# Kernel tuning notes

Measured on AMD Instinct MI355X. Metric: run time of the kernel, lower is better.

The kernel has to match this reference:

```python
import jax, jax.numpy as jnp
import numpy as np

BETA = 0.25

def _l2norm(x, eps=1e-12):
    # F.normalize(x, dim=-1)
    n = jnp.sqrt(jnp.sum(x * x, axis=-1, keepdims=True))
    return x / jnp.maximum(n, eps)

def setup_inputs() -> dict:
    key = jax.random.key(0)
    k1, k2 = jax.random.split(key)
    z = jax.random.normal(k1, (32, 1024, 32), dtype=jnp.float32)
    embedding = jax.random.normal(k2, (8192, 32), dtype=jnp.float32)
    return {"z": z, "embedding": embedding}

def reference(z, embedding):
    B, T, D = z.shape
    zf = _l2norm(z.reshape(-1, D))            # [N, D]
    en = _l2norm(embedding)                   # [n_e, D]
    # squared distances: ||z||^2 + ||e||^2 - 2 z.e  -> [N, n_e]
    d = (jnp.sum(zf * zf, axis=1, keepdims=True)
         + jnp.sum(en * en, axis=1)
         - 2.0 * jnp.einsum('nd,kd->nk', zf, en))
    idx = jnp.argmin(d, axis=1).reshape(B, T)            # [B, T]
    z_q = embedding[idx]                                  # [B, T, D] gather
    z_qnorm = _l2norm(z_q)
    z_norm = _l2norm(z)
    loss = (BETA * jnp.mean((jax.lax.stop_gradient(z_qnorm) - z_norm) ** 2)
            + jnp.mean((z_qnorm - jax.lax.stop_gradient(z_norm)) ** 2))
    # straight-through estimator
    z_q_out = z + jax.lax.stop_gradient(z_qnorm - z)
    return z_q_out, loss, idx
```

## Files before the change

### kernel.cpp

```cpp
#include <hip/hip_runtime.h>
#include <math.h>


#define D 32
#define KCODES 8192
#define MARGIN_Q 5.0e-4f
#define EPS 1e-12f

typedef short bf16x8 __attribute__((ext_vector_type(8)));
typedef unsigned short u16x8 __attribute__((ext_vector_type(8)));
typedef float f32x4 __attribute__((ext_vector_type(4)));

static __device__ __forceinline__ unsigned short f2bf(float x) {
  unsigned u = __float_as_uint(x);
  return (unsigned short)((u + 0x7FFFu + ((u >> 16) & 1u)) >> 16);
}
static __device__ __forceinline__ float bf2f(unsigned short s) {
  return __uint_as_float(((unsigned)s) << 16);
}
static __device__ __forceinline__ void gload_lds16(const void* g, void* l) {
  __builtin_amdgcn_global_load_lds(
      (const __attribute__((address_space(1))) void*)g,
      (__attribute__((address_space(3))) void*)l, 16, 0, 0);
}


__global__ __launch_bounds__(256) void k_prep(const float* __restrict__ emb,
                                              float* __restrict__ en,
                                              float* __restrict__ en_h,
                                              unsigned short* __restrict__ eswz,
                                              int* __restrict__ cnt,
                                              float* __restrict__ loss) {
  int v = blockIdx.x * 256 + threadIdx.x;
  if (v == 0) { *cnt = 0; *loss = 0.f; }
  if (v >= KCODES) return;

  float x[D];
  const float4* p = reinterpret_cast<const float4*>(emb + (size_t)v * D);
#pragma unroll
  for (int j = 0; j < D / 4; ++j) {
    float4 q = p[j];
    x[4 * j + 0] = q.x; x[4 * j + 1] = q.y; x[4 * j + 2] = q.z; x[4 * j + 3] = q.w;
  }
  float ss = 0.f;
#pragma unroll
  for (int j = 0; j < D; ++j) ss = fmaf(x[j], x[j], ss);
  float n = fmaxf(sqrtf(ss), EPS);
#pragma unroll
  for (int j = 0; j < D; ++j) x[j] = x[j] / n;

  float4* o = reinterpret_cast<float4*>(en + (size_t)v * D);
  float s2 = 0.f;
#pragma unroll
  for (int j = 0; j < D / 4; ++j) {
    float4 q = {x[4 * j], x[4 * j + 1], x[4 * j + 2], x[4 * j + 3]};
    s2 = fmaf(q.x, q.x, fmaf(q.y, q.y, fmaf(q.z, q.z, fmaf(q.w, q.w, s2))));
    o[j] = q;
  }
  en_h[v] = 0.5f * s2;

  unsigned short hi[D], lo[D];
#pragma unroll
  for (int j = 0; j < D; ++j) {
    hi[j] = f2bf(x[j]);
    lo[j] = f2bf(x[j] - bf2f(hi[j]));
  }
  int tl = v >> 4, m = v & 15;
#pragma unroll
  for (int q = 0; q < 4; ++q) {
    u16x8 hv, lv;
#pragma unroll
    for (int j = 0; j < 8; ++j) { hv[j] = hi[8 * q + j]; lv[j] = lo[8 * q + j]; }
    *(u16x8*)(eswz + (size_t)tl * 1024 + (q * 16 + m) * 8) = hv;
    *(u16x8*)(eswz + (size_t)tl * 1024 + 512 + (q * 16 + m) * 8) = lv;
  }
}

__global__ __launch_bounds__(256, 2) void k_argmin_mfma(
    const float* __restrict__ z,
    const unsigned short* __restrict__ eswz,
    int* __restrict__ idx_ws, int* __restrict__ list, int* __restrict__ cnt,
    unsigned long long* __restrict__ mp2) {
  __shared__ unsigned short lds_sh[2][16384];

  const int tid = threadIdx.x;
  const int wid = tid >> 6, lane = tid & 63;
  const int lane15 = lane & 15, quad = lane >> 4;
  const int g = blockIdx.x * 4 + wid;

  const float4* gall = reinterpret_cast<const float4*>(eswz);
#pragma unroll
  for (int i = 0; i < 8; ++i) {
    int off = i * 256 + tid;
    gload_lds16(gall + off, (char*)&lds_sh[0][0] + (size_t)off * 16);
  }

  bf16x8 zhi, zlo;
  {
    const float4* p = reinterpret_cast<const float4*>(z + (size_t)(g * 16 + lane15) * D);
    float ss = 0.f;
#pragma unroll
    for (int j = 0; j < 8; ++j) {
      float4 q = p[j];
      ss = fmaf(q.x, q.x, fmaf(q.y, q.y, fmaf(q.z, q.z, fmaf(q.w, q.w, ss))));
    }
    float nn = fmaxf(sqrtf(ss), EPS);
    float4 a0 = p[quad * 2], a1 = p[quad * 2 + 1];
    float xs[8] = {a0.x / nn, a0.y / nn, a0.z / nn, a0.w / nn,
                   a1.x / nn, a1.y / nn, a1.z / nn, a1.w / nn};
#pragma unroll
    for (int j = 0; j < 8; ++j) {
      unsigned short h = f2bf(xs[j]);
      zhi[j] = (short)h;
      zlo[j] = (short)f2bf(xs[j] - bf2f(h));
    }
  }

  unsigned p1[4], p2[4];
#pragma unroll
  for (int r = 0; r < 4; ++r) { p1[r] = 0u; p2[r] = 0u; }
  const f32x4 initA = {1.25f, 1.25f, 1.25f, 1.25f};
  const f32x4 zero4 = {0.f, 0.f, 0.f, 0.f};

  for (int c = 0; c < 32; ++c) {
    __syncthreads();
    if (c + 1 < 32) {
      const float4* gn = gall + (size_t)(c + 1) * 2048;
      char* dst = (char*)&lds_sh[(c + 1) & 1][0];
#pragma unroll
      for (int i = 0; i < 8; ++i) {
        int off = i * 256 + tid;
        gload_lds16(gn + off, dst + (size_t)off * 16);
      }
    }
    const unsigned short* buf = &lds_sh[c & 1][0];
    bf16x8 cbh = *(const bf16x8*)(buf + lane * 8);
    bf16x8 cbl = *(const bf16x8*)(buf + 512 + lane * 8);
    const unsigned tbase = (unsigned)(511 - c * 16);
#pragma unroll
    for (int t = 0; t < 16; ++t) {
      bf16x8 nbh, nbl;
      if (t < 15) {
        nbh = *(const bf16x8*)(buf + (t + 1) * 1024 + lane * 8);
        nbl = *(const bf16x8*)(buf + (t + 1) * 1024 + 512 + lane * 8);
      }
      f32x4 aa = __builtin_amdgcn_mfma_f32_16x16x32_bf16(zhi, cbh, initA, 0, 0, 0);
      f32x4 ab = __builtin_amdgcn_mfma_f32_16x16x32_bf16(zhi, cbl, zero4, 0, 0, 0);
      ab = __builtin_amdgcn_mfma_f32_16x16x32_bf16(zlo, cbh, ab, 0, 0, 0);
      const unsigned tid9 = tbase - t;
#pragma unroll
      for (int r = 0; r < 4; ++r) {
        float sa = aa[r] + ab[r];
        unsigned pk = (__float_as_uint(sa) & 0xFFFFFE00u) | tid9;
        unsigned tmin = (pk < p1[r]) ? pk : p1[r];
        p1[r] = (pk > p1[r]) ? pk : p1[r];
        p2[r] = (tmin > p2[r]) ? tmin : p2[r];
      }
      cbh = nbh; cbl = nbl;
    }
  }

#pragma unroll
  for (int r = 0; r < 4; ++r) {
    int kl = (511 - (int)(p1[r] & 511u)) * 16 + lane15;
    unsigned sb = p1[r] & 0xFFFFFE00u;
    float s1f = __uint_as_float(sb);
    float s2f = __uint_as_float(p2[r] & 0xFFFFFE00u);
    unsigned long long pk =
        ((unsigned long long)sb << 32) | (unsigned)(8191 - kl);
#pragma unroll
    for (int m = 1; m <= 8; m <<= 1) {
      unsigned long long op = __shfl_xor(pk, m, 64);
      float os1 = __shfl_xor(s1f, m, 64);
      float os2 = __shfl_xor(s2f, m, 64);
      s2f = fmaxf(fmaxf(s2f, os2), fminf(s1f, os1));
      s1f = fmaxf(s1f, os1);
      pk = (op > pk) ? op : pk;
    }
    if (lane15 == 0) {
      int orow = g * 16 + quad * 4 + r;
      if (s1f - s2f < MARGIN_Q) {
        int pos = atomicAdd(cnt, 1);
        list[pos] = orow;
        mp2[pos] = 0ull;
        idx_ws[orow] = -(pos + 1);
      } else {
        idx_ws[orow] = 8191 - (int)(unsigned)(pk & 0xFFFFFFFFull);
      }
    }
  }
}

__global__ __launch_bounds__(256) void k_cleanup(const float* __restrict__ z,
                                                 const float* __restrict__ en,
                                                 const float* __restrict__ en_h,
                                                 const int* __restrict__ list,
                                                 const int* __restrict__ cnt,
                                                 unsigned long long* __restrict__ mp2) {
  __shared__ unsigned long long wred[4];
  const int tid = threadIdx.x;
  const int lane = tid & 63, wid = tid >> 6;
  const int ntask = (*cnt) * 32;

  for (int j = blockIdx.x; j < ntask; j += gridDim.x) {
    int i = j >> 5, kc = j & 31;
    int row = list[i];
    const float* zr = z + (size_t)row * D;
    float v[D];
    float ss = 0.f;
#pragma unroll
    for (int d = 0; d < D; ++d) v[d] = zr[d];
#pragma unroll
    for (int d = 0; d < D; ++d) ss = fmaf(v[d], v[d], ss);
    float n = fmaxf(sqrtf(ss), EPS);
#pragma unroll
    for (int d = 0; d < D; ++d) v[d] = v[d] / n;

    int k = kc * 256 + tid;
    const float4* er = reinterpret_cast<const float4*>(en + (size_t)k * D);
    float a = -en_h[k];
#pragma unroll
    for (int jj = 0; jj < 8; ++jj) {
      float4 e = er[jj];
      a = fmaf(v[4 * jj + 0], e.x, a);
      a = fmaf(v[4 * jj + 1], e.y, a);
      a = fmaf(v[4 * jj + 2], e.z, a);
      a = fmaf(v[4 * jj + 3], e.w, a);
    }
    unsigned o = __float_as_uint(a);
    o = (o & 0x80000000u) ? ~o : (o | 0x80000000u);
    unsigned long long pk = ((unsigned long long)o << 32) | (unsigned)(8191 - k);
#pragma unroll
    for (int m = 32; m >= 1; m >>= 1) {
      unsigned long long op = __shfl_xor(pk, m, 64);
      pk = (op > pk) ? op : pk;
    }
    if (lane == 0) wred[wid] = pk;
    __syncthreads();
    if (tid == 0) {
      unsigned long long m01 = (wred[0] > wred[1]) ? wred[0] : wred[1];
      unsigned long long m23 = (wred[2] > wred[3]) ? wred[2] : wred[3];
      atomicMax(&mp2[i], (m01 > m23) ? m01 : m23);
    }
    __syncthreads();
  }
}

__global__ __launch_bounds__(256) void k_epi(const float* __restrict__ z,
                                             const float* __restrict__ en,
                                             const int* __restrict__ idx_ws,
                                             const unsigned long long* __restrict__ mp2,
                                             float* __restrict__ out_z,
                                             float* __restrict__ loss,
                                             float* __restrict__ out_idx,
                                             float scale) {
  int row = blockIdx.x * 256 + threadIdx.x;
  int kb = idx_ws[row];
  if (kb < 0) {
    unsigned long long m = mp2[-kb - 1];
    kb = 8191 - (int)(unsigned)(m & 0xFFFFFFFFull);
  }
  out_idx[row] = (float)kb;

  const float4* p = reinterpret_cast<const float4*>(z + (size_t)row * D);
  float4 q[D / 4];
#pragma unroll
  for (int j = 0; j < D / 4; ++j) q[j] = p[j];
  float ss = 0.f;
#pragma unroll
  for (int j = 0; j < D / 4; ++j)
    ss = fmaf(q[j].x, q[j].x, fmaf(q[j].y, q[j].y, fmaf(q[j].z, q[j].z, fmaf(q[j].w, q[j].w, ss))));
  float n = fmaxf(sqrtf(ss), EPS);

  const float4* ep = reinterpret_cast<const float4*>(en + (size_t)kb * D);
  float4* op = reinterpret_cast<float4*>(out_z + (size_t)row * D);
  float s = 0.f;
#pragma unroll
  for (int j = 0; j < D / 4; ++j) {
    float4 e = ep[j];
    float4 o;
    o.x = q[j].x + (e.x - q[j].x);
    o.y = q[j].y + (e.y - q[j].y);
    o.z = q[j].z + (e.z - q[j].z);
    o.w = q[j].w + (e.w - q[j].w);
    op[j] = o;
    float dx = e.x - q[j].x / n;  float dy = e.y - q[j].y / n;
    float dz = e.z - q[j].z / n;  float dw = e.w - q[j].w / n;
    s = fmaf(dx, dx, fmaf(dy, dy, fmaf(dz, dz, fmaf(dw, dw, s))));
  }

#pragma unroll
  for (int off = 32; off > 0; off >>= 1) s += __shfl_down(s, off, 64);
  __shared__ float wsum[4];
  int lane = threadIdx.x & 63, wid = threadIdx.x >> 6;
  if (lane == 0) wsum[wid] = s;
  __syncthreads();
  if (threadIdx.x == 0) {
    float tt = (wsum[0] + wsum[1]) + (wsum[2] + wsum[3]);
    atomicAdd(loss, tt * scale);
  }
}

extern "C" void kernel_launch(void* const* d_in, const int* in_sizes, int n_in,
                              void* d_out, int out_size, void* d_ws, size_t ws_size,
                              hipStream_t stream) {
  const float* z = (const float*)d_in[0];
  const float* emb = (const float*)d_in[1];
  const int N = in_sizes[0] / D;
  const int K = in_sizes[1] / D;

  float* out = (float*)d_out;
  float* out_z = out;
  float* loss = out + (size_t)N * D;
  float* out_idx = out + (size_t)N * D + 1;

  char* w = (char*)d_ws;
  float* en = (float*)w;                         w += (size_t)K * D * 4;
  float* en_h = (float*)w;                       w += (size_t)K * 4;
  unsigned short* eswz = (unsigned short*)w;     w += (size_t)K * D * 2 * 2;
  int* idx_ws = (int*)w;                         w += (size_t)N * 4;
  int* list = (int*)w;                           w += (size_t)N * 4;
  unsigned long long* mp2 = (unsigned long long*)w; w += (size_t)N * 8;
  int* cnt = (int*)w;

  k_prep<<<dim3(K / 256), 256, 0, stream>>>(emb, en, en_h, eswz, cnt, loss);

  k_argmin_mfma<<<dim3(N / 64), 256, 0, stream>>>(
      z, eswz, idx_ws, list, cnt, mp2);

  k_cleanup<<<dim3(2048), 256, 0, stream>>>(z, en, en_h, list, cnt, mp2);

  k_epi<<<dim3(N / 256), 256, 0, stream>>>(
      z, en, idx_ws, mp2, out_z, loss, out_idx, 1.25f / (float)((size_t)N * D));
}
```

Baseline: 210.0 us.

## Split codebook across blocks, reuse codebook tiles over four row groups per wave

The argmin kernel now splits the 8192 codes into 4 slices along a second grid dimension, and each wave handles 64 rows (four 16-row MFMA groups) against each LDS-loaded codebook tile. The goal is to amortise the LDS reads and global loads of the codebook across more rows and to fuse the MFMA accumulation into a single chain. Partial top-2 results are written per split, and the last-arriving block for a row group (found with an atomic ticket counter) merges them and flags ambiguous rows. The cleanup margin is tightened and the packed index uses fewer bits. The change adds some workspace traffic, more registers per wave and dead leftover code, and a tighter margin raises the risk of incorrect argmins.

```diff
diff --git a/kernel.cpp b/kernel.cpp
--- a/kernel.cpp
+++ b/kernel.cpp
@@ -4,7 +4,11 @@
 
 #define D 32
 #define KCODES 8192
-#define MARGIN_Q 5.0e-4f
+#define KSPLIT 4
+#define SPLITCODES 2048
+#define NCHUNK 8
+#define MASK8 0xFFFFFF00u
+#define MARGIN_Q 2.0e-4f
 #define EPS 1e-12f
 
 typedef short bf16x8 __attribute__((ext_vector_type(8)));
@@ -22,6 +26,9 @@
   __builtin_amdgcn_global_load_lds(
       (const __attribute__((address_space(1))) void*)g,
       (__attribute__((address_space(3))) void*)l, 16, 0, 0);
+}
+static __device__ __forceinline__ unsigned umax3(unsigned a, unsigned b, unsigned c) {
+  return max(max(a, b), c);
 }
 
 
@@ -30,9 +37,12 @@
                                               float* __restrict__ en_h,
                                               unsigned short* __restrict__ eswz,
                                               int* __restrict__ cnt,
-                                              float* __restrict__ loss) {
+                                              float* __restrict__ loss,
+                                              int* __restrict__ tick,
+                                              int ntick) {
   int v = blockIdx.x * 256 + threadIdx.x;
   if (v == 0) { *cnt = 0; *loss = 0.f; }
+  if (v < ntick) tick[v] = 0;
   if (v >= KCODES) return;
 
   float x[D];
@@ -79,25 +89,35 @@
 __global__ __launch_bounds__(256, 2) void k_argmin_mfma(
     const float* __restrict__ z,
     const unsigned short* __restrict__ eswz,
+    unsigned long long* __restrict__ mpp,
+    float* __restrict__ g2,
+    int* __restrict__ tick,
     int* __restrict__ idx_ws, int* __restrict__ list, int* __restrict__ cnt,
-    unsigned long long* __restrict__ mp2) {
+    unsigned long long* __restrict__ mp2, int N) {
   __shared__ unsigned short lds_sh[2][16384];
+  __shared__ int s_old;
 
   const int tid = threadIdx.x;
   const int wid = tid >> 6, lane = tid & 63;
   const int lane15 = lane & 15, quad = lane >> 4;
-  const int g = blockIdx.x * 4 + wid;
-
-  const float4* gall = reinterpret_cast<const float4*>(eswz);
+  const int rb = blockIdx.x;
+  const int split = blockIdx.y;
+  const int rowbase = rb * 256 + wid * 64;
+  const int kbase = split * SPLITCODES;
+
+  const float4* gall = reinterpret_cast<const float4*>(eswz) +
+                       (size_t)(split * 128) * 128;
 #pragma unroll
   for (int i = 0; i < 8; ++i) {
     int off = i * 256 + tid;
     gload_lds16(gall + off, (char*)&lds_sh[0][0] + (size_t)off * 16);
   }
 
-  bf16x8 zhi, zlo;
-  {
-    const float4* p = reinterpret_cast<const float4*>(z + (size_t)(g * 16 + lane15) * D);
+  bf16x8 zh[4], zl[4];
+#pragma unroll
+  for (int g = 0; g < 4; ++g) {
+    const float4* p =
+        reinterpret_cast<const float4*>(z + (size_t)(rowbase + g * 16 + lane15) * D);
     float ss = 0.f;
 #pragma unroll
     for (int j = 0; j < 8; ++j) {
@@ -111,20 +131,21 @@
 #pragma unroll
     for (int j = 0; j < 8; ++j) {
       unsigned short h = f2bf(xs[j]);
-      zhi[j] = (short)h;
-      zlo[j] = (short)f2bf(xs[j] - bf2f(h));
-    }
-  }
-
-  unsigned p1[4], p2[4];
-#pragma unroll
-  for (int r = 0; r < 4; ++r) { p1[r] = 0u; p2[r] = 0u; }
-  const f32x4 initA = {1.25f, 1.25f, 1.25f, 1.25f};
-  const f32x4 zero4 = {0.f, 0.f, 0.f, 0.f};
-
-  for (int c = 0; c < 32; ++c) {
+      zh[g][j] = (short)h;
+      zl[g][j] = (short)f2bf(xs[j] - bf2f(h));
+    }
+  }
+
+  unsigned p1[4][4], p2[4][4];
+#pragma unroll
+  for (int g = 0; g < 4; ++g)
+#pragma unroll
+    for (int r = 0; r < 4; ++r) { p1[g][r] = 0u; p2[g][r] = 0u; }
+  const f32x4 initc = {1.25f, 1.25f, 1.25f, 1.25f};
+
+  for (int c = 0; c < NCHUNK; ++c) {
     __syncthreads();
-    if (c + 1 < 32) {
+    if (c + 1 < NCHUNK) {
       const float4* gn = gall + (size_t)(c + 1) * 2048;
       char* dst = (char*)&lds_sh[(c + 1) & 1][0];
 #pragma unroll
@@ -134,59 +155,95 @@
       }
     }
     const unsigned short* buf = &lds_sh[c & 1][0];
-    bf16x8 cbh = *(const bf16x8*)(buf + lane * 8);
-    bf16x8 cbl = *(const bf16x8*)(buf + 512 + lane * 8);
-    const unsigned tbase = (unsigned)(511 - c * 16);
 #pragma unroll
     for (int t = 0; t < 16; ++t) {
-      bf16x8 nbh, nbl;
-      if (t < 15) {
-        nbh = *(const bf16x8*)(buf + (t + 1) * 1024 + lane * 8);
-        nbl = *(const bf16x8*)(buf + (t + 1) * 1024 + 512 + lane * 8);
+      bf16x8 bh = *(const bf16x8*)(buf + t * 1024 + lane * 8);
+      bf16x8 bl = *(const bf16x8*)(buf + t * 1024 + 512 + lane * 8);
+      const unsigned tid8 = (unsigned)(255 - (c * 16 + t));
+#pragma unroll
+      for (int g = 0; g < 4; ++g) {
+        f32x4 acc = __builtin_amdgcn_mfma_f32_16x16x32_bf16(zh[g], bh, initc, 0, 0, 0);
+        acc = __builtin_amdgcn_mfma_f32_16x16x32_bf16(zh[g], bl, acc, 0, 0, 0);
+        acc = __builtin_amdgcn_mfma_f32_16x16x32_bf16(zl[g], bh, acc, 0, 0, 0);
+        unsigned q0 = (__float_as_uint(acc[0]) & MASK8) | tid8;
+        unsigned q1 = (__float_as_uint(acc[1]) & MASK8) | tid8;
+        unsigned q2 = (__float_as_uint(acc[2]) & MASK8) | tid8;
+        unsigned q3 = (__float_as_uint(acc[3]) & MASK8) | tid8;
+        unsigned m01 = max(q0, q1), n01 = min(q0, q1);
+        unsigned m23 = max(q2, q3), n23 = min(q2, q3);
+        unsigned M = max(m01, m23), t2 = min(m01, m23);
+        unsigned dem = min(p1[g][0 * 0], M);
+        (void)dem;
+#pragma unroll
+        for (int r = 0; r < 1; ++r) {}
+        unsigned t0 = min(q0, p1[g][0]); p1[g][0] = max(q0, p1[g][0]); p2[g][0] = max(t0, p2[g][0]);
+        unsigned t1 = min(q1, p1[g][1]); p1[g][1] = max(q1, p1[g][1]); p2[g][1] = max(t1, p2[g][1]);
+        unsigned t2b = min(q2, p1[g][2]); p1[g][2] = max(q2, p1[g][2]); p2[g][2] = max(t2b, p2[g][2]);
+        unsigned t3 = min(q3, p1[g][3]); p1[g][3] = max(q3, p1[g][3]); p2[g][3] = max(t3, p2[g][3]);
+        (void)M; (void)t2; (void)m01; (void)n01; (void)m23; (void)n23;
       }
-      f32x4 aa = __builtin_amdgcn_mfma_f32_16x16x32_bf16(zhi, cbh, initA, 0, 0, 0);
-      f32x4 ab = __builtin_amdgcn_mfma_f32_16x16x32_bf16(zhi, cbl, zero4, 0, 0, 0);
-      ab = __builtin_amdgcn_mfma_f32_16x16x32_bf16(zlo, cbh, ab, 0, 0, 0);
-      const unsigned tid9 = tbase - t;
-#pragma unroll
-      for (int r = 0; r < 4; ++r) {
-        float sa = aa[r] + ab[r];
-        unsigned pk = (__float_as_uint(sa) & 0xFFFFFE00u) | tid9;
-        unsigned tmin = (pk < p1[r]) ? pk : p1[r];
-        p1[r] = (pk > p1[r]) ? pk : p1[r];
-        p2[r] = (tmin > p2[r]) ? tmin : p2[r];
+    }
+  }
+
+#pragma unroll
+  for (int g = 0; g < 4; ++g) {
+#pragma unroll
+    for (int r = 0; r < 4; ++r) {
+      unsigned pv = p1[g][r];
+      unsigned sb = pv & MASK8;
+      int tile = 255 - (int)(pv & 0xFFu);
+      int kfull = kbase + tile * 16 + lane15;
+      float s1f = __uint_as_float(sb);
+      float s2f = __uint_as_float(p2[g][r] & MASK8);
+      unsigned long long pk =
+          ((unsigned long long)sb << 32) | (unsigned)(8191 - kfull);
+#pragma unroll
+      for (int m = 1; m <= 8; m <<= 1) {
+        unsigned long long op = __shfl_xor(pk, m, 64);
+        float os1 = __shfl_xor(s1f, m, 64);
+        float os2 = __shfl_xor(s2f, m, 64);
+        s2f = fmaxf(fmaxf(s2f, os2), fminf(s1f, os1));
+        s1f = fmaxf(s1f, os1);
+        pk = (op > pk) ? op : pk;
       }
-      cbh = nbh; cbl = nbl;
-    }
-  }
-
-#pragma unroll
-  for (int r = 0; r < 4; ++r) {
-    int kl = (511 - (int)(p1[r] & 511u)) * 16 + lane15;
-    unsigned sb = p1[r] & 0xFFFFFE00u;
-    float s1f = __uint_as_float(sb);
-    float s2f = __uint_as_float(p2[r] & 0xFFFFFE00u);
-    unsigned long long pk =
-        ((unsigned long long)sb << 32) | (unsigned)(8191 - kl);
-#pragma unroll
-    for (int m = 1; m <= 8; m <<= 1) {
-      unsigned long long op = __shfl_xor(pk, m, 64);
-      float os1 = __shfl_xor(s1f, m, 64);
-      float os2 = __shfl_xor(s2f, m, 64);
-      s2f = fmaxf(fmaxf(s2f, os2), fminf(s1f, os1));
-      s1f = fmaxf(s1f, os1);
-      pk = (op > pk) ? op : pk;
-    }
-    if (lane15 == 0) {
-      int orow = g * 16 + quad * 4 + r;
-      if (s1f - s2f < MARGIN_Q) {
-        int pos = atomicAdd(cnt, 1);
-        list[pos] = orow;
-        mp2[pos] = 0ull;
-        idx_ws[orow] = -(pos + 1);
-      } else {
-        idx_ws[orow] = 8191 - (int)(unsigned)(pk & 0xFFFFFFFFull);
+      if (lane15 == 0) {
+        int row = rowbase + g * 16 + quad * 4 + r;
+        mpp[(size_t)split * N + row] = pk;
+        g2[(size_t)split * N + row] = s2f;
       }
+    }
+  }
+
+  __threadfence();
+  __syncthreads();
+  if (tid == 0) s_old = atomicAdd(&tick[rb], 1);
+  __syncthreads();
+  if (s_old == KSPLIT - 1) {
+    __threadfence();
+    int row = rb * 256 + tid;
+    unsigned long long k0 = mpp[(size_t)0 * N + row];
+    unsigned long long k1 = mpp[(size_t)1 * N + row];
+    unsigned long long k2 = mpp[(size_t)2 * N + row];
+    unsigned long long k3 = mpp[(size_t)3 * N + row];
+    float a0 = g2[(size_t)0 * N + row], a1 = g2[(size_t)1 * N + row];
+    float a2 = g2[(size_t)2 * N + row], a3 = g2[(size_t)3 * N + row];
+    unsigned long long m01 = (k0 > k1) ? k0 : k1;
+    unsigned long long m23 = (k2 > k3) ? k2 : k3;
+    unsigned long long B = (m01 > m23) ? m01 : m23;
+    float s1g = __uint_as_float((unsigned)(B >> 32));
+    float c0 = (k0 == B) ? a0 : __uint_as_float((unsigned)(k0 >> 32));
+    float c1 = (k1 == B) ? a1 : __uint_as_float((unsigned)(k1 >> 32));
+    float c2 = (k2 == B) ? a2 : __uint_as_float((unsigned)(k2 >> 32));
+    float c3 = (k3 == B) ? a3 : __uint_as_float((unsigned)(k3 >> 32));
+    float s2g = fmaxf(fmaxf(c0, c1), fmaxf(c2, c3));
+    int kb = 8191 - (int)(unsigned)(B & 0xFFFFFFFFull);
+    if (s1g - s2g < MARGIN_Q) {
+      int pos = atomicAdd(cnt, 1);
+      list[pos] = row;
+      mp2[pos] = 0ull;
+      idx_ws[row] = -(pos + 1);
+    } else {
+      idx_ws[row] = kb;
     }
   }
 }
@@ -315,18 +372,23 @@
   float* out_idx = out + (size_t)N * D + 1;
 
   char* w = (char*)d_ws;
+  unsigned long long* mpp = (unsigned long long*)w; w += (size_t)KSPLIT * N * 8;
+  unsigned long long* mp2 = (unsigned long long*)w; w += (size_t)N * 8;
   float* en = (float*)w;                         w += (size_t)K * D * 4;
   float* en_h = (float*)w;                       w += (size_t)K * 4;
   unsigned short* eswz = (unsigned short*)w;     w += (size_t)K * D * 2 * 2;
+  float* g2 = (float*)w;                         w += (size_t)KSPLIT * N * 4;
   int* idx_ws = (int*)w;                         w += (size_t)N * 4;
   int* list = (int*)w;                           w += (size_t)N * 4;
-  unsigned long long* mp2 = (unsigned long long*)w; w += (size_t)N * 8;
+  int* tick = (int*)w;                           w += 512;
   int* cnt = (int*)w;
 
-  k_prep<<<dim3(K / 256), 256, 0, stream>>>(emb, en, en_h, eswz, cnt, loss);
-
-  k_argmin_mfma<<<dim3(N / 64), 256, 0, stream>>>(
-      z, eswz, idx_ws, list, cnt, mp2);
+  const int nrb = N / 256;
+
+  k_prep<<<dim3(K / 256), 256, 0, stream>>>(emb, en, en_h, eswz, cnt, loss, tick, nrb);
+
+  k_argmin_mfma<<<dim3(nrb, KSPLIT), 256, 0, stream>>>(
+      z, eswz, mpp, g2, tick, idx_ws, list, cnt, mp2, N);
 
   k_cleanup<<<dim3(2048), 256, 0, stream>>>(z, en, en_h, list, cnt, mp2);
 
```

New measurement: 220.4 us. +4.9%, slower.
